# Optimization experiments

Measured on AMD Instinct MI355X. Metric: run time of the kernel, lower is better.

## Reference

```python
import jax, jax.numpy as jnp
import numpy as np

ROPE_BASE = 10000.0

def rotary_pe_3d(x, coords):
    # x: [B, H, L, D]; coords: [B, L, 3]. Split D into 3 axis chunks; rotate
    # each chunk (half-split pairs) by angles coord_axis * inv_freq.
    D = x.shape[-1]
    da = D // 3            # dims per spatial axis
    p = da // 2            # rotary pairs per axis
    inv_freq = 1.0 / (ROPE_BASE ** (jnp.arange(p, dtype=x.dtype) / p))  # [p]
    chunks = []
    for a in range(3):
        xa = x[..., a * da:(a + 1) * da]                       # [B,H,L,da]
        theta = coords[..., a][:, None, :, None] * inv_freq    # [B,1,L,p]
        cos, sin = jnp.cos(theta), jnp.sin(theta)
        x1, x2 = xa[..., :p], xa[..., p:]
        chunks.append(jnp.concatenate([x1 * cos - x2 * sin,
                                       x1 * sin + x2 * cos], axis=-1))
    if 3 * da < D:  # leave any remainder un-rotated
        chunks.append(x[..., 3 * da:])
    return jnp.concatenate(chunks, axis=-1)


def setup_inputs() -> dict:
    key = jax.random.key(0)
    ks = jax.random.split(key, 16)
    B, Lq, Lk, D, H = 4, 1024, 4096, 768, 8
    s = 1.0 / np.sqrt(D)
    return {
        "query": jax.random.normal(ks[0], (B, Lq, D), jnp.float32),
        "key": jax.random.normal(ks[1], (B, Lk, D), jnp.float32),
        "value": jax.random.normal(ks[2], (B, Lk, D), jnp.float32),
        "coords_query": jax.random.normal(ks[3], (B, Lq, 3), jnp.float32),
        "coords_key": jax.random.normal(ks[4], (B, Lk, 3), jnp.float32),
        "Wq": jax.random.normal(ks[5], (D, D), jnp.float32) * s,
        "bq": jnp.zeros((D,), jnp.float32),
        "Wk": jax.random.normal(ks[6], (D, D), jnp.float32) * s,
        "bk": jnp.zeros((D,), jnp.float32),
        "Wv": jax.random.normal(ks[7], (D, D), jnp.float32) * s,
        "bv": jnp.zeros((D,), jnp.float32),
        "Wo": jax.random.normal(ks[8], (D, D), jnp.float32) * s,
        "bo": jnp.zeros((D,), jnp.float32),
    }


def reference(query, key, value, coords_query, coords_key,
              Wq, bq, Wk, bk, Wv, bv, Wo, bo):
    B, Lq, D = query.shape
    Lk = key.shape[1]
    H = 8
    hd = D // H
    # Projections (nn.Linear: x @ W.T + b)
    q = (query @ Wq.T + bq).reshape(B, Lq, H, hd).transpose(0, 2, 1, 3)  # [B,H,Lq,hd]
    k = (key @ Wk.T + bk).reshape(B, Lk, H, hd).transpose(0, 2, 1, 3)
    v = (value @ Wv.T + bv).reshape(B, Lk, H, hd).transpose(0, 2, 1, 3)
    q = rotary_pe_3d(q, coords_query)
    k = rotary_pe_3d(k, coords_key)
    scores = jnp.einsum("bhqd,bhkd->bhqk", q, k) / jnp.sqrt(jnp.asarray(hd, q.dtype))
    attn = jax.nn.softmax(scores, axis=-1)  # dropout is identity in eval
    out = jnp.einsum("bhqk,bhkd->bhqd", attn, v)
    out = out.transpose(0, 2, 1, 3).reshape(B, Lq, D)
    return out @ Wo.T + bo
```

## Files before the change

kernel.cpp:

```cpp
#include <hip/hip_runtime.h>
#include <math.h>

#define DM 768
#define NH 8
#define HD 96
#define BQ 4
#define LQ 1024
#define LK 4096
#define BH (BQ*NH)
#define KVS 4
#define KC (LK/KVS)
#define NT (KC/64)
#define QB 128
#define NW (DM*DM)
#define NKSTEP (DM/64)

typedef unsigned short ushort;
typedef unsigned int uint;
typedef __attribute__((ext_vector_type(8))) short short8v;
typedef __attribute__((ext_vector_type(4))) float float4v;

#define QSCALE 0.14724444641f

static __device__ __forceinline__ ushort f2bf(float x) {
    union { float f; uint u; } c; c.f = x;
    uint u = c.u;
    u += ((u >> 16) & 1u) + 0x7fffu;
    return (ushort)(u >> 16);
}

static __device__ __forceinline__ float bf2f(ushort x) {
    union { uint u; float f; } c; c.u = (uint)x << 16;
    return c.f;
}

static __device__ __forceinline__ uint cvtpk(float lo, float hi) {
    uint d;
    asm("v_cvt_pk_bf16_f32 %0, %1, %2" : "=v"(d) : "v"(lo), "v"(hi));
    return d;
}

static __device__ __forceinline__ float exp2hw(float x) {
#if __has_builtin(__builtin_amdgcn_exp2f)
    return __builtin_amdgcn_exp2f(x);
#else
    return __expf(x * 0.6931471805599453f);
#endif
}

static __device__ __forceinline__ void gload_lds16(const void* g, void* l) {
    __builtin_amdgcn_global_load_lds(
        (const __attribute__((address_space(1))) uint*)g,
        (__attribute__((address_space(3))) uint*)l, 16, 0, 0);
}

__global__ __launch_bounds__(256)
void wcvt(const float* __restrict__ w0, const float* __restrict__ w1,
          const float* __restrict__ w2, const float* __restrict__ w3,
          ushort* __restrict__ d)
{
    const int SEG = NW / 1024;
    int b = blockIdx.x;
    int wsel = b / SEG, ib = b % SEG;
    const float* s = (wsel == 0) ? w0 : (wsel == 1) ? w1 : (wsel == 2) ? w2 : w3;
    int i = ib * 256 + threadIdx.x;
    float4 v = ((const float4*)s)[i];
    uint2 o;
    o.x = (uint)f2bf(v.x) | ((uint)f2bf(v.y) << 16);
    o.y = (uint)f2bf(v.z) | ((uint)f2bf(v.w) << 16);
    ((uint2*)(d + (size_t)wsel * NW))[i] = o;
}

__global__ __launch_bounds__(256, 2)
void qkv_gemm(const float* __restrict__ qf, const float* __restrict__ kf,
              const float* __restrict__ vf,
              const ushort* __restrict__ wqb, const ushort* __restrict__ wkb,
              const ushort* __restrict__ wvb,
              const float* __restrict__ bq, const float* __restrict__ bk,
              const float* __restrict__ bv,
              const float* __restrict__ cq, const float* __restrict__ ck,
              ushort* __restrict__ qws, ushort* __restrict__ kws,
              ushort* __restrict__ vtb)
{
    __shared__ ushort Sh[24576];
    char* As = (char*)Sh;
    char* Bs = (char*)Sh + 16384;

    const int tid  = threadIdx.x;
    const int w    = tid >> 6;
    const int lane = tid & 63;
    const int l15  = lane & 15;
    const int lg   = lane >> 4;
    const int wm   = w >> 1, wn = w & 1;

    const int L = blockIdx.x;
    int seg, idx, Lshift, rpx;
    const float* X32; const ushort* Wbp; const float* bias; const float* coords;
    ushort* out; float oscale;
    if (L < 96)       { seg = 0; idx = L;       X32 = qf; Wbp = wqb; bias = bq; coords = cq; out = qws; Lshift = 10; rpx = 4;  oscale = QSCALE; }
    else if (L < 480) { seg = 1; idx = L - 96;  X32 = kf; Wbp = wkb; bias = bk; coords = ck; out = kws; Lshift = 12; rpx = 16; oscale = 1.0f; }
    else              { seg = 2; idx = L - 480; X32 = vf; Wbp = wvb; bias = bv; coords = 0;  out = vtb; Lshift = 12; rpx = 16; oscale = 1.0f; }

    const int xcd  = idx & 7;
    const int sq   = idx >> 3;
    const int col0 = (sq % 3) * 256;
    const int row0 = (xcd * rpx + sq / 3) * 128;

    float4v acc[4][8];
    #pragma unroll
    for (int m = 0; m < 4; ++m)
        #pragma unroll
        for (int n = 0; n < 8; ++n) acc[m][n] = (float4v)0.f;

    int PA[4], rA[4], cA[4];
    #pragma unroll
    for (int c = 0; c < 4; ++c) {
        int P = ((w*4 + c) << 10) + lane*16;
        int lgc = P ^ (((P >> 9) & 3) << 5);
        PA[c] = P;
        rA[c] = lgc >> 7;
        cA[c] = (lgc & 127) >> 1;
    }
    int PB[8], rB[8], cB[8];
    #pragma unroll
    for (int c = 0; c < 8; ++c) {
        int P = ((w*8 + c) << 10) + lane*16;
        int lgc = P ^ (((P >> 9) & 3) << 5);
        PB[c] = P;
        rB[c] = lgc >> 7;
        cB[c] = (lgc & 127) >> 1;
    }
    const float*  xb = X32 + (size_t)row0 * DM;
    const ushort* wb = Wbp + (size_t)col0 * DM;

    int offA[2][4], offB[2][8];
    #pragma unroll
    for (int kk = 0; kk < 2; ++kk) {
        #pragma unroll
        for (int m = 0; m < 4; ++m) {
            int byte = (wm*64 + m*16 + l15)*128 + kk*64 + lg*16;
            offA[kk][m] = byte ^ (((byte >> 9) & 3) << 5);
        }
        #pragma unroll
        for (int n = 0; n < 8; ++n) {
            int byte = (wn*128 + n*16 + l15)*128 + kk*64 + lg*16;
            offB[kk][n] = byte ^ (((byte >> 9) & 3) << 5);
        }
    }

    for (int kt = 0; kt < DM; kt += 64) {
        #pragma unroll
        for (int c = 0; c < 8; ++c)
            gload_lds16(wb + (size_t)rB[c]*DM + kt + cB[c], Bs + PB[c]);
        float4 fa[4], fb[4];
        #pragma unroll
        for (int c = 0; c < 4; ++c) {
            const float* src = xb + (size_t)rA[c]*DM + kt + cA[c];
            fa[c] = *(const float4*)src;
            fb[c] = *(const float4*)(src + 4);
        }
        #pragma unroll
        for (int c = 0; c < 4; ++c) {
            uint4 pk;
            pk.x = cvtpk(fa[c].x, fa[c].y);
            pk.y = cvtpk(fa[c].z, fa[c].w);
            pk.z = cvtpk(fb[c].x, fb[c].y);
            pk.w = cvtpk(fb[c].z, fb[c].w);
            *(uint4*)(As + PA[c]) = pk;
        }
        __syncthreads();
        #pragma unroll
        for (int kk = 0; kk < 2; ++kk) {
            short8v af[4], bfm[8];
            #pragma unroll
            for (int m = 0; m < 4; ++m)
                af[m] = *(const short8v*)(As + offA[kk][m]);
            #pragma unroll
            for (int n = 0; n < 8; ++n)
                bfm[n] = *(const short8v*)(Bs + offB[kk][n]);
            #pragma unroll
            for (int m = 0; m < 4; ++m)
                #pragma unroll
                for (int n = 0; n < 8; ++n)
                    acc[m][n] = __builtin_amdgcn_mfma_f32_16x16x32_bf16(af[m], bfm[n], acc[m][n], 0, 0, 0);
        }
        __syncthreads();
    }

    const int colbase = col0 + wn*128;
    float bvv[8];
    #pragma unroll
    for (int nt = 0; nt < 8; ++nt) bvv[nt] = bias[colbase + nt*16 + l15];
    #pragma unroll
    for (int m = 0; m < 4; ++m)
        #pragma unroll
        for (int nt = 0; nt < 8; ++nt)
            #pragma unroll
            for (int r = 0; r < 4; ++r) acc[m][nt][r] += bvv[nt];

    if (seg < 2) {
        const float freq = exp2f(-(float)l15 * 0.83048202372184058696f);
        int ap[4];
        #pragma unroll
        for (int p = 0; p < 4; ++p) ap[p] = ((colbase >> 5) + p) % 3;
        #pragma unroll
        for (int m = 0; m < 4; ++m) {
            #pragma unroll
            for (int r = 0; r < 4; ++r) {
                int row = row0 + wm*64 + m*16 + lg*4 + r;
                const float* c3 = coords + (size_t)row * 3;
                #pragma unroll
                for (int p = 0; p < 4; ++p) {
                    float sn, cs;
                    __sincosf(c3[ap[p]] * freq, &sn, &cs);
                    float A_ = acc[m][2*p][r], B_ = acc[m][2*p+1][r];
                    acc[m][2*p][r]   = (A_*cs - B_*sn) * oscale;
                    acc[m][2*p+1][r] = (A_*sn + B_*cs) * oscale;
                }
            }
        }
        const int Lm1 = (1 << Lshift) - 1;
        int hh[8], tt[8];
        #pragma unroll
        for (int nt = 0; nt < 8; ++nt) {
            int j0 = colbase + nt*16;
            hh[nt] = j0 / HD;
            tt[nt] = j0 % HD + l15;
        }
        #pragma unroll
        for (int m = 0; m < 4; ++m)
            #pragma unroll
            for (int r = 0; r < 4; ++r) {
                int row = row0 + wm*64 + m*16 + lg*4 + r;
                int b = row >> Lshift, l = row & Lm1;
                #pragma unroll
                for (int nt = 0; nt < 8; ++nt)
                    out[(((size_t)b*NH + hh[nt]) << Lshift | l) * HD + tt[nt]] =
                        f2bf(acc[m][nt][r]);
            }
    } else {
        #pragma unroll
        for (int h2 = 0; h2 < 2; ++h2) {
            __syncthreads();
            if (wn == h2) {
                #pragma unroll
                for (int m = 0; m < 4; ++m)
                    #pragma unroll
                    for (int nt = 0; nt < 8; ++nt)
                        #pragma unroll
                        for (int r = 0; r < 4; ++r) {
                            int c  = nt*16 + l15;
                            int ri = wm*64 + m*16 + lg*4 + r;
                            *(ushort*)((char*)Sh + c*256 + (((ri>>3) ^ (c&7))<<4) + (ri&7)*2)
                                = f2bf(acc[m][nt][r]);
                        }
            }
            __syncthreads();
            #pragma unroll
            for (int e = 0; e < 8; ++e) {
                int idx2 = tid + 256*e;
                int c = idx2 >> 4, r8 = idx2 & 15;
                uint4 val = *(const uint4*)((const char*)Sh + c*256 + ((r8 ^ (c&7))<<4));
                int j = col0 + h2*128 + c;
                int h = j / HD, t = j % HD;
                int row = row0 + r8*8;
                int b = row >> 12, l = row & (LK-1);
                *(uint4*)&out[(((size_t)b*NH + h)*HD + t)*LK + l] = val;
            }
        }
    }
}

__global__ __launch_bounds__(256)
void gemm_out(const ushort* __restrict__ X, const ushort* __restrict__ Wb,
              const float* __restrict__ bias, float* __restrict__ out)
{
    __shared__ ushort Sh[16384];
    char* As = (char*)Sh;
    char* Bs = (char*)Sh + 16384;

    const int tid  = threadIdx.x;
    const int w    = tid >> 6;
    const int lane = tid & 63;
    const int l15  = lane & 15;
    const int lg   = lane >> 4;
    const int wm   = w >> 1, wn = w & 1;

    const int L    = blockIdx.x;
    const int xcd  = L & 7;
    const int sq   = L >> 3;
    const int col0 = (sq % 6) * 128;
    const int row0 = (xcd * 4 + sq / 6) * 128;

    float4v acc[4][4];
    #pragma unroll
    for (int m = 0; m < 4; ++m)
        #pragma unroll
        for (int n = 0; n < 4; ++n) acc[m][n] = (float4v)0.f;

    int Pp[4], rrS[4], cbS[4];
    #pragma unroll
    for (int c = 0; c < 4; ++c) {
        int P = ((w*4 + c) << 10) + lane*16;
        int lgc = P ^ (((P >> 9) & 3) << 5);
        Pp[c]  = P;
        rrS[c] = lgc >> 7;
        cbS[c] = (lgc & 127) >> 1;
    }
    const ushort* xb = X  + (size_t)row0 * DM;
    const ushort* wb = Wb + (size_t)col0 * DM;

    int offA[2][4], offB[2][4];
    #pragma unroll
    for (int kk = 0; kk < 2; ++kk) {
        #pragma unroll
        for (int m = 0; m < 4; ++m) {
            int byte = (wm*64 + m*16 + l15)*128 + kk*64 + lg*16;
            offA[kk][m] = byte ^ (((byte >> 9) & 3) << 5);
            byte = (wn*64 + m*16 + l15)*128 + kk*64 + lg*16;
            offB[kk][m] = byte ^ (((byte >> 9) & 3) << 5);
        }
    }

    for (int kt = 0; kt < DM; kt += 64) {
        #pragma unroll
        for (int c = 0; c < 4; ++c) {
            gload_lds16(xb + (size_t)rrS[c]*DM + kt + cbS[c], As + Pp[c]);
            gload_lds16(wb + (size_t)rrS[c]*DM + kt + cbS[c], Bs + Pp[c]);
        }
        __syncthreads();
        #pragma unroll
        for (int kk = 0; kk < 2; ++kk) {
            short8v af[4], bfm[4];
            #pragma unroll
            for (int m = 0; m < 4; ++m)
                af[m] = *(const short8v*)(As + offA[kk][m]);
            #pragma unroll
            for (int n = 0; n < 4; ++n)
                bfm[n] = *(const short8v*)(Bs + offB[kk][n]);
            #pragma unroll
            for (int m = 0; m < 4; ++m)
                #pragma unroll
                for (int n = 0; n < 4; ++n)
                    acc[m][n] = __builtin_amdgcn_mfma_f32_16x16x32_bf16(af[m], bfm[n], acc[m][n], 0, 0, 0);
        }
        __syncthreads();
    }

    const int colbase = col0 + wn*64;
    float bvv[4];
    #pragma unroll
    for (int nt = 0; nt < 4; ++nt) bvv[nt] = bias[colbase + nt*16 + l15];
    #pragma unroll
    for (int m = 0; m < 4; ++m)
        #pragma unroll
        for (int r = 0; r < 4; ++r) {
            int row = row0 + wm*64 + m*16 + lg*4 + r;
            #pragma unroll
            for (int nt = 0; nt < 4; ++nt)
                out[(size_t)row*DM + colbase + nt*16 + l15] = acc[m][nt][r] + bvv[nt];
        }
}

__global__ __launch_bounds__(256, 2)
void attn_mfma(const ushort* __restrict__ q, const ushort* __restrict__ k,
               const ushort* __restrict__ vt, ushort* __restrict__ opb,
               float* __restrict__ mlb)
{
    __shared__ ushort Ks[64*128];
    __shared__ ushort Vs[96*64];
    __shared__ ushort PsT[4][32][72];

    const int tid  = threadIdx.x;
    const int w    = tid >> 6;
    const int lane = tid & 63;
    const int l15  = lane & 15;
    const int lg   = lane >> 4;

    const int L   = blockIdx.x;
    const int xcd = L & 7;
    const int s   = L >> 3;
    const int pr  = xcd*16 + (s >> 3);
    const int qt  = s & 7;
    const int bh  = pr & 31;
    const int sc  = pr >> 5;

    const ushort* qg = q  + ((size_t)bh * LQ + qt*QB + w*32 + l15) * HD;
    const ushort* kg = k  + ((size_t)bh * LK + (size_t)sc * KC) * HD;
    const ushort* vg = vt + (size_t)bh * HD * LK + (size_t)sc * KC;

    short8v aq0[3], aq1[3];
    #pragma unroll
    for (int dc = 0; dc < 3; ++dc) {
        aq0[dc] = *(const short8v*)(qg + dc*32 + lg*8);
        aq1[dc] = *(const short8v*)(qg + 16*HD + dc*32 + lg*8);
    }

    int kdst[3], ksrc[3], vdst[3], vsrc[3];
    #pragma unroll
    for (int j = 0; j < 3; ++j) {
        int c = tid + 256*j;
        int kr = c / 12, ks = c % 12;
        kdst[j] = kr*256 + ((ks ^ (kr & 7)) << 4);
        ksrc[j] = kr*HD + ks*8;
        int vr = c >> 3, vs = c & 7;
        vdst[j] = vr*128 + ((vs ^ (vr & 7)) << 4);
        vsrc[j] = vr*LK + vs*8;
    }
    int tK[3], tV[2];
    #pragma unroll
    for (int dc = 0; dc < 3; ++dc) tK[dc] = ((dc*4 + lg) ^ (l15 & 7)) << 4;
    #pragma unroll
    for (int h2 = 0; h2 < 2; ++h2)  tV[h2] = ((h2*4 + lg) ^ (l15 & 7)) << 4;

    float4v o0[6], o1[6];
    #pragma unroll
    for (int dt = 0; dt < 6; ++dt) { o0[dt] = (float4v)0.f; o1[dt] = (float4v)0.f; }
    float m_0 = -1e30f, l_0 = 0.f;
    float m_1 = -1e30f, l_1 = 0.f;

    short8v kreg[3], vreg[3];
    #pragma unroll
    for (int j = 0; j < 3; ++j) {
        kreg[j] = *(const short8v*)(kg + ksrc[j]);
        vreg[j] = *(const short8v*)(vg + vsrc[j]);
    }
    #pragma unroll
    for (int j = 0; j < 3; ++j) {
        *(short8v*)((char*)Ks + kdst[j]) = kreg[j];
        *(short8v*)((char*)Vs + vdst[j]) = vreg[j];
    }
    __syncthreads();

    for (int t = 0; t < NT; ++t) {
        if (t + 1 < NT) {
            const ushort* kn = kg + (size_t)(t+1)*64*HD;
            const ushort* vn = vg + (t+1)*64;
            #pragma unroll
            for (int j = 0; j < 3; ++j) {
                kreg[j] = *(const short8v*)(kn + ksrc[j]);
                vreg[j] = *(const short8v*)(vn + vsrc[j]);
            }
        }

        float4v s0[4], s1[4];
        __builtin_amdgcn_s_setprio(1);
        #pragma unroll
        for (int nt = 0; nt < 4; ++nt) {
            s0[nt] = (float4v)0.f;
            s1[nt] = (float4v)0.f;
            #pragma unroll
            for (int dc = 0; dc < 3; ++dc) {
                short8v bk = *(const short8v*)((const char*)Ks + nt*4096 + l15*256 + tK[dc]);
                s0[nt] = __builtin_amdgcn_mfma_f32_16x16x32_bf16(bk, aq0[dc], s0[nt], 0, 0, 0);
                s1[nt] = __builtin_amdgcn_mfma_f32_16x16x32_bf16(bk, aq1[dc], s1[nt], 0, 0, 0);
            }
        }
        __builtin_amdgcn_s_setprio(0);

        float mt0 = -1e30f, mt1 = -1e30f;
        #pragma unroll
        for (int nt = 0; nt < 4; ++nt)
            #pragma unroll
            for (int r = 0; r < 4; ++r) {
                mt0 = fmaxf(mt0, s0[nt][r]);
                mt1 = fmaxf(mt1, s1[nt][r]);
            }
        mt0 = fmaxf(mt0, __shfl_xor(mt0, 16, 64));
        mt0 = fmaxf(mt0, __shfl_xor(mt0, 32, 64));
        mt1 = fmaxf(mt1, __shfl_xor(mt1, 16, 64));
        mt1 = fmaxf(mt1, __shfl_xor(mt1, 32, 64));

        if (__any((mt0 > m_0 + 11.5f) || (mt1 > m_1 + 11.5f))) {
            float mn0 = fmaxf(m_0, mt0), mn1 = fmaxf(m_1, mt1);
            float a0 = exp2hw(m_0 - mn0), a1 = exp2hw(m_1 - mn1);
            m_0 = mn0; m_1 = mn1;
            l_0 *= a0;  l_1 *= a1;
            float al0[4], al1[4];
            #pragma unroll
            for (int r = 0; r < 4; ++r) {
                al0[r] = __shfl(a0, lg*4 + r, 64);
                al1[r] = __shfl(a1, lg*4 + r, 64);
            }
            #pragma unroll
            for (int dt = 0; dt < 6; ++dt)
                #pragma unroll
                for (int r = 0; r < 4; ++r) {
                    o0[dt][r] *= al0[r];
                    o1[dt][r] *= al1[r];
                }
        }

        float ps0 = 0.f, ps1 = 0.f;
        #pragma unroll
        for (int nt = 0; nt < 4; ++nt)
            #pragma unroll
            for (int r = 0; r < 4; ++r) {
                float p0 = exp2hw(s0[nt][r] - m_0);
                float p1 = exp2hw(s1[nt][r] - m_1);
                s0[nt][r] = p0; ps0 += p0;
                s1[nt][r] = p1; ps1 += p1;
            }
        ps0 += __shfl_xor(ps0, 16, 64);
        ps0 += __shfl_xor(ps0, 32, 64);
        ps1 += __shfl_xor(ps1, 16, 64);
        ps1 += __shfl_xor(ps1, 32, 64);
        l_0 += ps0;
        l_1 += ps1;

        #pragma unroll
        for (int nt = 0; nt < 4; ++nt) {
            uint2 pk0, pk1;
            pk0.x = cvtpk(s0[nt][0], s0[nt][1]);
            pk0.y = cvtpk(s0[nt][2], s0[nt][3]);
            pk1.x = cvtpk(s1[nt][0], s1[nt][1]);
            pk1.y = cvtpk(s1[nt][2], s1[nt][3]);
            *(uint2*)&PsT[w][l15][nt*16 + lg*4]      = pk0;
            *(uint2*)&PsT[w][16 + l15][nt*16 + lg*4] = pk1;
        }

        short8v a00 = *(const short8v*)&PsT[w][l15][lg*8];
        short8v a01 = *(const short8v*)&PsT[w][l15][32 + lg*8];
        short8v a10 = *(const short8v*)&PsT[w][16 + l15][lg*8];
        short8v a11 = *(const short8v*)&PsT[w][16 + l15][32 + lg*8];
        __builtin_amdgcn_s_setprio(1);
        #pragma unroll
        for (int dt = 0; dt < 6; ++dt) {
            short8v bv0 = *(const short8v*)((const char*)Vs + dt*2048 + l15*128 + tV[0]);
            short8v bv1 = *(const short8v*)((const char*)Vs + dt*2048 + l15*128 + tV[1]);
            o0[dt] = __builtin_amdgcn_mfma_f32_16x16x32_bf16(a00, bv0, o0[dt], 0, 0, 0);
            o0[dt] = __builtin_amdgcn_mfma_f32_16x16x32_bf16(a01, bv1, o0[dt], 0, 0, 0);
            o1[dt] = __builtin_amdgcn_mfma_f32_16x16x32_bf16(a10, bv0, o1[dt], 0, 0, 0);
            o1[dt] = __builtin_amdgcn_mfma_f32_16x16x32_bf16(a11, bv1, o1[dt], 0, 0, 0);
        }
        __builtin_amdgcn_s_setprio(0);
        __syncthreads();

        if (t + 1 < NT) {
            #pragma unroll
            for (int j = 0; j < 3; ++j) {
                *(short8v*)((char*)Ks + kdst[j]) = kreg[j];
                *(short8v*)((char*)Vs + vdst[j]) = vreg[j];
            }
        }
        __syncthreads();
    }

    ushort* ob = opb + (((size_t)sc * BH + bh) * LQ + qt*QB + w*32) * HD;
    #pragma unroll
    for (int r = 0; r < 4; ++r) {
        #pragma unroll
        for (int dt = 0; dt < 6; ++dt) {
            ob[(size_t)(lg*4 + r) * HD + dt*16 + l15]      = f2bf(o0[dt][r]);
            ob[(size_t)(16 + lg*4 + r) * HD + dt*16 + l15] = f2bf(o1[dt][r]);
        }
    }
    if (lane < 16) {
        size_t mlrow = ((size_t)sc * BH + bh) * LQ + qt*QB + w*32 + lane;
        mlb[mlrow*2 + 0] = m_0;
        mlb[mlrow*2 + 1] = l_0;
        mlb[(mlrow + 16)*2 + 0] = m_1;
        mlb[(mlrow + 16)*2 + 1] = l_1;
    }
}

__global__ __launch_bounds__(256)
void combine(const ushort* __restrict__ opb, const float* __restrict__ mlb,
             ushort* __restrict__ ctx)
{
    const int NROW = BH * LQ;
    int idx = blockIdx.x * 256 + threadIdx.x;
    int row = idx / 12, seg = idx % 12;

    float m[KVS], lv[KVS];
    #pragma unroll
    for (int i = 0; i < KVS; ++i) {
        m[i]  = mlb[((size_t)i*NROW + row)*2 + 0];
        lv[i] = mlb[((size_t)i*NROW + row)*2 + 1];
    }
    float ms = m[0];
    #pragma unroll
    for (int i = 1; i < KVS; ++i) ms = fmaxf(ms, m[i]);
    float wsum = 0.f, wgt[KVS];
    #pragma unroll
    for (int i = 0; i < KVS; ++i) {
        wgt[i] = exp2hw(m[i] - ms);
        wsum += lv[i] * wgt[i];
    }
    float inv = 1.f / wsum;

    float acc[8] = {};
    #pragma unroll
    for (int i = 0; i < KVS; ++i) {
        uint4 v = *(const uint4*)&opb[((size_t)i*NROW + row)*HD + seg*8];
        uint vv[4] = {v.x, v.y, v.z, v.w};
        #pragma unroll
        for (int j2 = 0; j2 < 4; ++j2) {
            acc[j2*2+0] += bf2f((ushort)(vv[j2] & 0xffff)) * wgt[i];
            acc[j2*2+1] += bf2f((ushort)(vv[j2] >> 16))    * wgt[i];
        }
    }

    int bh = row / LQ, l = row % LQ;
    int b = bh >> 3, h = bh & 7;
    ushort* o = ctx + ((size_t)b * LQ + l) * DM + h * HD + seg*8;
    uint4 pk;
    pk.x = cvtpk(acc[0]*inv, acc[1]*inv);
    pk.y = cvtpk(acc[2]*inv, acc[3]*inv);
    pk.z = cvtpk(acc[4]*inv, acc[5]*inv);
    pk.w = cvtpk(acc[6]*inv, acc[7]*inv);
    *(uint4*)o = pk;
}

extern "C" void kernel_launch(void* const* d_in, const int* in_sizes, int n_in,
                              void* d_out, int out_size, void* d_ws, size_t ws_size,
                              hipStream_t stream)
{
    const float* query = (const float*)d_in[0];
    const float* key   = (const float*)d_in[1];
    const float* value = (const float*)d_in[2];
    const float* cq    = (const float*)d_in[3];
    const float* ck    = (const float*)d_in[4];
    const float* Wq    = (const float*)d_in[5];
    const float* bqv   = (const float*)d_in[6];
    const float* Wk    = (const float*)d_in[7];
    const float* bkv   = (const float*)d_in[8];
    const float* Wv    = (const float*)d_in[9];
    const float* bvv   = (const float*)d_in[10];
    const float* Wo    = (const float*)d_in[11];
    const float* bov   = (const float*)d_in[12];
    float* out = (float*)d_out;

    const size_t NQ = (size_t)BQ * LQ * DM;
    const size_t NK = (size_t)BQ * LK * DM;
    const size_t NP = (size_t)KVS * BH * LQ * HD;

    ushort* wq  = (ushort*)d_ws;
    ushort* wk  = wq  + NW;
    ushort* wv  = wk  + NW;
    ushort* wo  = wv  + NW;
    ushort* qws = wo  + NW;
    ushort* kws = qws + NQ;
    ushort* vtb = kws + NK;
    ushort* opb = vtb + NK;
    ushort* ctx = opb + NP;
    float*  mlb = (float*)(ctx + NQ);

    wcvt<<<4*(NW/1024), 256, 0, stream>>>(Wq, Wk, Wv, Wo, wq);
    qkv_gemm<<<864, 256, 0, stream>>>(query, key, value, wq, wk, wv,
                                      bqv, bkv, bvv, cq, ck, qws, kws, vtb);
    attn_mfma<<<(LQ/QB) * BH * KVS, 256, 0, stream>>>(qws, kws, vtb, opb, mlb);
    combine<<<BH*LQ*12/256, 256, 0, stream>>>(opb, mlb, ctx);
    gemm_out<<<(BQ*LQ/128)*6, 256, 0, stream>>>(ctx, wo, bov, out);
}
```

Baseline: 170.9 us.

## Register-prefetch next K tile in QKV GEMM and halve out-proj row tile

In the QKV projection GEMM, the loads for the next K step (fp32 activations and bf16 weights) now go into registers during the current step's MFMA work, then are converted and written to LDS after a barrier. This replaces the async global-to-LDS path with a software pipeline, hiding global load latency at the cost of more registers and an extra barrier per step. The output projection GEMM moves from 128-row to 64-row tiles, which doubles the grid and allows 4 blocks per CU, so occupancy on the small final GEMM goes up. The tradeoff is that weight tiles are reloaded more often.

```diff
diff --git a/kernel.cpp b/kernel.cpp
--- a/kernel.cpp
+++ b/kernel.cpp
@@ -148,27 +148,44 @@
         }
     }
 
-    for (int kt = 0; kt < DM; kt += 64) {
-        #pragma unroll
-        for (int c = 0; c < 8; ++c)
-            gload_lds16(wb + (size_t)rB[c]*DM + kt + cB[c], Bs + PB[c]);
-        float4 fa[4], fb[4];
-        #pragma unroll
-        for (int c = 0; c < 4; ++c) {
-            const float* src = xb + (size_t)rA[c]*DM + kt + cA[c];
-            fa[c] = *(const float4*)src;
-            fb[c] = *(const float4*)(src + 4);
-        }
-        #pragma unroll
-        for (int c = 0; c < 4; ++c) {
-            uint4 pk;
-            pk.x = cvtpk(fa[c].x, fa[c].y);
-            pk.y = cvtpk(fa[c].z, fa[c].w);
-            pk.z = cvtpk(fb[c].x, fb[c].y);
-            pk.w = cvtpk(fb[c].z, fb[c].w);
-            *(uint4*)(As + PA[c]) = pk;
-        }
-        __syncthreads();
+    float4 fa[4], fb[4];
+    short8v bregs[8];
+    #pragma unroll
+    for (int c = 0; c < 4; ++c) {
+        const float* src = xb + (size_t)rA[c]*DM + cA[c];
+        fa[c] = *(const float4*)src;
+        fb[c] = *(const float4*)(src + 4);
+    }
+    #pragma unroll
+    for (int c = 0; c < 8; ++c)
+        bregs[c] = *(const short8v*)(wb + (size_t)rB[c]*DM + cB[c]);
+    #pragma unroll
+    for (int c = 0; c < 4; ++c) {
+        uint4 pk;
+        pk.x = cvtpk(fa[c].x, fa[c].y);
+        pk.y = cvtpk(fa[c].z, fa[c].w);
+        pk.z = cvtpk(fb[c].x, fb[c].y);
+        pk.w = cvtpk(fb[c].z, fb[c].w);
+        *(uint4*)(As + PA[c]) = pk;
+    }
+    #pragma unroll
+    for (int c = 0; c < 8; ++c)
+        *(short8v*)(Bs + PB[c]) = bregs[c];
+    __syncthreads();
+
+    for (int t = 0; t < NKSTEP; ++t) {
+        if (t + 1 < NKSTEP) {
+            const int kn = (t + 1) * 64;
+            #pragma unroll
+            for (int c = 0; c < 4; ++c) {
+                const float* src = xb + (size_t)rA[c]*DM + kn + cA[c];
+                fa[c] = *(const float4*)src;
+                fb[c] = *(const float4*)(src + 4);
+            }
+            #pragma unroll
+            for (int c = 0; c < 8; ++c)
+                bregs[c] = *(const short8v*)(wb + (size_t)rB[c]*DM + kn + cB[c]);
+        }
         #pragma unroll
         for (int kk = 0; kk < 2; ++kk) {
             short8v af[4], bfm[8];
@@ -183,6 +200,21 @@
                 #pragma unroll
                 for (int n = 0; n < 8; ++n)
                     acc[m][n] = __builtin_amdgcn_mfma_f32_16x16x32_bf16(af[m], bfm[n], acc[m][n], 0, 0, 0);
+        }
+        __syncthreads();
+        if (t + 1 < NKSTEP) {
+            #pragma unroll
+            for (int c = 0; c < 4; ++c) {
+                uint4 pk;
+                pk.x = cvtpk(fa[c].x, fa[c].y);
+                pk.y = cvtpk(fa[c].z, fa[c].w);
+                pk.z = cvtpk(fb[c].x, fb[c].y);
+                pk.w = cvtpk(fb[c].z, fb[c].w);
+                *(uint4*)(As + PA[c]) = pk;
+            }
+            #pragma unroll
+            for (int c = 0; c < 8; ++c)
+                *(short8v*)(Bs + PB[c]) = bregs[c];
         }
         __syncthreads();
     }
@@ -271,13 +303,13 @@
     }
 }
 
-__global__ __launch_bounds__(256)
+__global__ __launch_bounds__(256, 4)
 void gemm_out(const ushort* __restrict__ X, const ushort* __restrict__ Wb,
               const float* __restrict__ bias, float* __restrict__ out)
 {
-    __shared__ ushort Sh[16384];
+    __shared__ ushort Sh[12288];
     char* As = (char*)Sh;
-    char* Bs = (char*)Sh + 16384;
+    char* Bs = (char*)Sh + 8192;
 
     const int tid  = threadIdx.x;
     const int w    = tid >> 6;
@@ -290,56 +322,69 @@
     const int xcd  = L & 7;
     const int sq   = L >> 3;
     const int col0 = (sq % 6) * 128;
-    const int row0 = (xcd * 4 + sq / 6) * 128;
-
-    float4v acc[4][4];
-    #pragma unroll
-    for (int m = 0; m < 4; ++m)
+    const int row0 = (xcd * 8 + sq / 6) * 64;
+
+    float4v acc[2][4];
+    #pragma unroll
+    for (int m = 0; m < 2; ++m)
         #pragma unroll
         for (int n = 0; n < 4; ++n) acc[m][n] = (float4v)0.f;
 
-    int Pp[4], rrS[4], cbS[4];
+    int PA[2], rA[2], cA[2];
+    #pragma unroll
+    for (int c = 0; c < 2; ++c) {
+        int P = ((w*2 + c) << 10) + lane*16;
+        int lgc = P ^ (((P >> 9) & 3) << 5);
+        PA[c] = P;
+        rA[c] = lgc >> 7;
+        cA[c] = (lgc & 127) >> 1;
+    }
+    int PB[4], rB[4], cB[4];
     #pragma unroll
     for (int c = 0; c < 4; ++c) {
         int P = ((w*4 + c) << 10) + lane*16;
         int lgc = P ^ (((P >> 9) & 3) << 5);
-        Pp[c]  = P;
-        rrS[c] = lgc >> 7;
-        cbS[c] = (lgc & 127) >> 1;
+        PB[c] = P;
+        rB[c] = lgc >> 7;
+        cB[c] = (lgc & 127) >> 1;
     }
     const ushort* xb = X  + (size_t)row0 * DM;
     const ushort* wb = Wb + (size_t)col0 * DM;
 
-    int offA[2][4], offB[2][4];
+    int offA[2][2], offB[2][4];
     #pragma unroll
     for (int kk = 0; kk < 2; ++kk) {
         #pragma unroll
-        for (int m = 0; m < 4; ++m) {
-            int byte = (wm*64 + m*16 + l15)*128 + kk*64 + lg*16;
+        for (int m = 0; m < 2; ++m) {
+            int byte = (wm*32 + m*16 + l15)*128 + kk*64 + lg*16;
             offA[kk][m] = byte ^ (((byte >> 9) & 3) << 5);
-            byte = (wn*64 + m*16 + l15)*128 + kk*64 + lg*16;
-            offB[kk][m] = byte ^ (((byte >> 9) & 3) << 5);
+        }
+        #pragma unroll
+        for (int n = 0; n < 4; ++n) {
+            int byte = (wn*64 + n*16 + l15)*128 + kk*64 + lg*16;
+            offB[kk][n] = byte ^ (((byte >> 9) & 3) << 5);
         }
     }
 
     for (int kt = 0; kt < DM; kt += 64) {
         #pragma unroll
-        for (int c = 0; c < 4; ++c) {
-            gload_lds16(xb + (size_t)rrS[c]*DM + kt + cbS[c], As + Pp[c]);
-            gload_lds16(wb + (size_t)rrS[c]*DM + kt + cbS[c], Bs + Pp[c]);
-        }
+        for (int c = 0; c < 2; ++c)
+            gload_lds16(xb + (size_t)rA[c]*DM + kt + cA[c], As + PA[c]);
+        #pragma unroll
+        for (int c = 0; c < 4; ++c)
+            gload_lds16(wb + (size_t)rB[c]*DM + kt + cB[c], Bs + PB[c]);
         __syncthreads();
         #pragma unroll
         for (int kk = 0; kk < 2; ++kk) {
-            short8v af[4], bfm[4];
-            #pragma unroll
-            for (int m = 0; m < 4; ++m)
+            short8v af[2], bfm[4];
+            #pragma unroll
+            for (int m = 0; m < 2; ++m)
                 af[m] = *(const short8v*)(As + offA[kk][m]);
             #pragma unroll
             for (int n = 0; n < 4; ++n)
                 bfm[n] = *(const short8v*)(Bs + offB[kk][n]);
             #pragma unroll
-            for (int m = 0; m < 4; ++m)
+            for (int m = 0; m < 2; ++m)
                 #pragma unroll
                 for (int n = 0; n < 4; ++n)
                     acc[m][n] = __builtin_amdgcn_mfma_f32_16x16x32_bf16(af[m], bfm[n], acc[m][n], 0, 0, 0);
@@ -352,10 +397,10 @@
     #pragma unroll
     for (int nt = 0; nt < 4; ++nt) bvv[nt] = bias[colbase + nt*16 + l15];
     #pragma unroll
-    for (int m = 0; m < 4; ++m)
+    for (int m = 0; m < 2; ++m)
         #pragma unroll
         for (int r = 0; r < 4; ++r) {
-            int row = row0 + wm*64 + m*16 + lg*4 + r;
+            int row = row0 + wm*32 + m*16 + lg*4 + r;
             #pragma unroll
             for (int nt = 0; nt < 4; ++nt)
                 out[(size_t)row*DM + colbase + nt*16 + l15] = acc[m][nt][r] + bvv[nt];
@@ -651,5 +696,5 @@
                                       bqv, bkv, bvv, cq, ck, qws, kws, vtb);
     attn_mfma<<<(LQ/QB) * BH * KVS, 256, 0, stream>>>(qws, kws, vtb, opb, mlb);
     combine<<<BH*LQ*12/256, 256, 0, stream>>>(opb, mlb, ctx);
-    gemm_out<<<(BQ*LQ/128)*6, 256, 0, stream>>>(ctx, wo, bov, out);
-}
+    gemm_out<<<(BQ*LQ/64)*6, 256, 0, stream>>>(ctx, wo, bov, out);
+}
```

Result: no change. 171.7 us (+0.5%).
